# Optimization experiments

Hardware: AMD Instinct MI355X
Metric: run time of the kernel (lower is better)

## Reference

```python
import jax, jax.numpy as jnp
import numpy as np

H = 512
W = 512
TEMP = 256.0
B, S = 4, 4096
C = 2 * H + 2 * W  # pred class dim


def setup_inputs() -> dict:
    key = jax.random.key(0)
    k1, k2, k3, k4, k5 = jax.random.split(key, 5)
    pred = jax.random.normal(k1, (B, S, C), jnp.float32)
    # target columns: [timestamp (sorted), h index, w index, polarity]
    times = jnp.sort(jax.random.uniform(k2, (B, S), jnp.float32, 0.0, 1.0e5), axis=1)
    h_idx = jax.random.randint(k3, (B, S), 0, H).astype(jnp.float32)
    w_idx = jax.random.randint(k4, (B, S), 0, W).astype(jnp.float32)
    p = jax.random.bernoulli(k5, 0.5, (B, S)).astype(jnp.float32)
    target = jnp.stack([times, h_idx, w_idx, p], axis=-1)  # [B,S,4]
    return {"pred": pred, "target": target}


def _soft_ce(pred_logits, tgt_logits):
    # CrossEntropyLoss with soft (probability) targets, reduction='none' -> [B,S]
    return -jnp.sum(jax.nn.softmax(tgt_logits, axis=-1) * jax.nn.log_softmax(pred_logits, axis=-1), axis=-1)


def reference(pred, target):
    t = target[:, :, 0]                      # [B,S] timestamps
    h = target[:, :, 1].astype(jnp.int32)    # [B,S] H indices
    w = target[:, :, 2].astype(jnp.int32)    # [B,S] W indices
    p = target[:, :, 3]                      # [B,S] polarity in {0,1}

    b_ix = jnp.arange(B)[:, None]
    s_ix = jnp.arange(S)[None, :]
    # scatter one-hot targets into a single [B,S,2H+2W] buffer (4 disjoint segments)
    a = jnp.zeros((B, S, C), pred.dtype)
    a = a.at[b_ix, s_ix, h].set(1.0 - p)             # H_0 segment [0,H)
    a = a.at[b_ix, s_ix, H + h].set(p)               # H_1 segment [H,2H)
    a = a.at[b_ix, s_ix, 2 * H + w].set(1.0 - p)     # W_0 segment [2H,2H+W)
    a = a.at[b_ix, s_ix, 2 * H + W + w].set(p)       # W_1 segment [2H+W,2H+2W)

    # decay[j] = exp(-(t[j+1]-t[j])/T); pad last step (unused, carry starts at 0)
    decay = jnp.exp(-(t[:, 1:] - t[:, :-1]) / TEMP)             # [B,S-1]
    decay = jnp.concatenate([decay, jnp.zeros((B, 1), decay.dtype)], axis=1)  # [B,S]

    # reverse linear recurrence: r[j] = a[j] + decay[j] * r[j+1]
    a_t = jnp.swapaxes(a, 0, 1)                 # [S,B,C]
    d_t = jnp.swapaxes(decay, 0, 1)[:, :, None]  # [S,B,1]

    def step(carry, xs):
        ai, di = xs
        r = ai + di * carry
        return r, r

    _, r = jax.lax.scan(step, jnp.zeros((B, C), pred.dtype), (a_t, d_t), reverse=True)
    r = jnp.swapaxes(r, 0, 1)                   # [B,S,C]
    # torch loop is range(S-1, 1, -1): index 0 is never accumulated into
    r = r.at[:, 0, :].set(a[:, 0, :])

    lH0 = _soft_ce(pred[:, :, :H], r[:, :, :H])
    lH1 = _soft_ce(pred[:, :, H:2 * H], r[:, :, H:2 * H])
    lW0 = _soft_ce(pred[:, :, 2 * H:2 * H + W], r[:, :, 2 * H:2 * H + W])
    lW1 = _soft_ce(pred[:, :, 2 * H + W:], r[:, :, 2 * H + W:])

    loss = ((lH0 + lW0) * (1.0 - p) + (lH1 + lW1) * p).mean()
    return loss
```

## Files before the change

kernel.cpp:

```cpp
#include <hip/hip_runtime.h>
#include <math.h>

#define NC 2048
#define NB 4
#define NS 4096
#define INV_TEMP (1.0f / 256.0f)
#define LOG2E 1.44269504088896340736f
#define CL 16
#define NCH (NS / CL)
#define P1_NG 16
#define P1_GS (NS / P1_NG)
#define P1_GC (P1_GS / CL)
#define LOSS_NBLK (NB * NCH)

typedef float f32x4 __attribute__((ext_vector_type(4)));
typedef float f32x2 __attribute__((ext_vector_type(2)));

#define WAVE_SUM_DPP(x)                                                       \
    asm volatile("s_nop 1\n\t"                                                \
                 "v_add_f32 %0, %0, %0 row_shr:1 bound_ctrl:0" : "+v"(x));    \
    asm volatile("s_nop 1\n\t"                                                \
                 "v_add_f32 %0, %0, %0 row_shr:2 bound_ctrl:0" : "+v"(x));    \
    asm volatile("s_nop 1\n\t"                                                \
                 "v_add_f32 %0, %0, %0 row_shr:4 bound_ctrl:0" : "+v"(x));    \
    asm volatile("s_nop 1\n\t"                                                \
                 "v_add_f32 %0, %0, %0 row_shr:8 bound_ctrl:0" : "+v"(x));    \
    asm volatile("s_nop 1\n\t"                                                \
                 "v_add_f32 %0, %0, %0 row_bcast:15 row_mask:0xa" : "+v"(x)); \
    asm volatile("s_nop 1\n\t"                                                \
                 "v_add_f32 %0, %0, %0 row_bcast:31 row_mask:0xc" : "+v"(x));

__device__ __forceinline__ float wave_total(float x)
{
    return __uint_as_float(__builtin_amdgcn_readlane(__float_as_uint(x), 63));
}

__global__ __launch_bounds__(512) void tdl_scan_kernel(
    const float* __restrict__ target, float* __restrict__ rstart)
{
    const int b     = blockIdx.x >> 6;
    const int ctile = blockIdx.x & 63;
    const int tid = threadIdx.x;
    const int ci  = tid & 31;
    const int g   = tid >> 5;

    __shared__ float shbuf[NS * 4];
    __shared__ float shL[P1_NG][32];
    __shared__ float shG[P1_NG];
    f32x4* ev = (f32x4*)shbuf;
    f32x2* pk = (f32x2*)shbuf;

    const int  seg    = ctile >> 4;
    const bool useH   = (seg < 2);
    const float segPar = (float)(seg & 1);
    const float crel  = (float)(((ctile & 15) << 5) + ci);

    const float* tb = target + (size_t)b * NS * 4;

#pragma unroll
    for (int m = 0; m < 8; ++m) {
        int s = m * 512 + tid;
        ev[s] = *((const f32x4*)tb + s);
    }
    __syncthreads();

    float dec_r[8], enc_r[8];
#pragma unroll
    for (int m = 0; m < 8; ++m) {
        int s = m * 512 + tid;
        f32x4 e = ev[s];
        dec_r[m] = (s == NS - 1) ? 0.0f
                  : __expf(-(ev[s + 1].x - e.x) * INV_TEMP);
        enc_r[m] = (e.w == segPar) ? (useH ? e.y : e.z) : -1.0f;
    }
    float alp[P1_GC];
    {
        const int gs = g * P1_GS;
#pragma unroll
        for (int q = 0; q < P1_GC; ++q) {
            int se = gs + q * CL;
            alp[q] = (g == P1_NG - 1 && q == P1_GC - 1) ? 0.0f
                     : __expf(-(ev[se + CL].x - ev[se].x) * INV_TEMP);
        }
        if (ci == 0) {
            shG[g] = (g == P1_NG - 1) ? 0.0f
                     : __expf(-(ev[gs + P1_GS].x - ev[gs].x) * INV_TEMP);
        }
    }
    __syncthreads();

#pragma unroll
    for (int m = 0; m < 8; ++m) {
        int s = m * 512 + tid;
        f32x2 v; v.x = dec_r[m]; v.y = enc_r[m];
        pk[s] = v;
    }
    __syncthreads();

    float cs[P1_GC];
    {
        const int gs = g * P1_GS;
#pragma unroll
        for (int q = P1_GC - 1; q >= 0; --q) {
            float v = 0.0f;
            const int base = gs + q * CL;
#pragma unroll
            for (int i = CL - 1; i >= 0; --i) {
                f32x2 e = pk[base + i];
                v = fmaf(v, e.x, (e.y == crel) ? 1.0f : 0.0f);
            }
            cs[q] = v;
        }
    }

    float L = 0.0f;
#pragma unroll
    for (int q = P1_GC - 1; q >= 0; --q) L = fmaf(alp[q], L, cs[q]);
    shL[g][ci] = L;
    __syncthreads();

    float X = 0.0f;
#pragma unroll
    for (int j = P1_NG - 1; j >= 1; --j)
        if (j > g) X = fmaf(shG[j], X, shL[j][ci]);

    float* rs = rstart + ((size_t)b * NCH + g * P1_GC) * NC + (ctile * 32 + ci);
    float carry = X;
#pragma unroll
    for (int q = P1_GC - 1; q >= 0; --q) {
        carry = fmaf(alp[q], carry, cs[q]);
        rs[(size_t)q * NC] = carry;
    }
}

__global__ __launch_bounds__(256) void tdl_loss_kernel(
    const float* __restrict__ pred, const float* __restrict__ target,
    const float* __restrict__ rstart, float* __restrict__ partials)
{
    const int blk = blockIdx.x;
    const int b = blk >> 8;
    const int k = blk & (NCH - 1);
    const int s0 = k * CL;
    const int tid = threadIdx.x;
    const int wv  = (tid >> 6) & 1;
    const int rh  = tid >> 7;
    const int ln  = tid & 63;

    __shared__ f32x4 ev[CL];
    __shared__ float sh4[4];

    if (tid < CL) {
        const float* tg = target + ((size_t)b * NS + s0 + tid) * 4;
        float t0 = tg[0];
        int s = s0 + tid;
        float dec = (s == NS - 1 || s == 0) ? 0.0f
                   : __expf(-(tg[4] - t0) * INV_TEMP);
        f32x4 e; e.x = dec; e.y = tg[3]; e.z = tg[1]; e.w = tg[2];
        ev[tid] = e;
    }
    __syncthreads();

    const int lc   = ln * 4;
    const int segA = wv * 2;
    const size_t pbase = (size_t)b * NS * NC;

    float vA[8], vB[8];
    if (k == NCH - 1) {
#pragma unroll
        for (int j = 0; j < 8; ++j) { vA[j] = 0.0f; vB[j] = 0.0f; }
    } else {
        const float* rrow = rstart + ((size_t)b * NCH + k + 1) * NC;
#pragma unroll
        for (int q = 0; q < 2; ++q) {
            f32x4 ra = *(const f32x4*)(rrow + segA * 512 + q * 256 + lc);
            f32x4 rb = *(const f32x4*)(rrow + (segA + 1) * 512 + q * 256 + lc);
#pragma unroll
            for (int j = 0; j < 4; ++j) {
                vA[q*4+j] = ra[j] * LOG2E;
                vB[q*4+j] = rb[j] * LOG2E;
            }
        }
    }

    if (rh) {
#pragma unroll
        for (int i = CL - 1; i >= CL / 2; --i) {
            f32x4 e = ev[i];
            const float d    = e.x;
            const float pv   = e.y;
            const float idxf = wv ? e.w : e.z;
            const float aA = (1.0f - pv) * LOG2E;
            const float aB = pv * LOG2E;
#pragma unroll
            for (int q = 0; q < 2; ++q) {
#pragma unroll
                for (int j = 0; j < 4; ++j) {
                    const int id = q * 4 + j;
                    const float myc = (float)(q * 256 + lc + j);
                    const bool m = (idxf == myc);
                    vA[id] = fmaf(vA[id], d, m ? aA : 0.0f);
                    vB[id] = fmaf(vB[id], d, m ? aB : 0.0f);
                }
            }
        }
    }

    const int itop = rh ? (CL / 2 - 1) : (CL - 1);

    f32x4 pf0[2], pf1[2];
    {
        const int paT = (int)ev[itop].y;
        const float* pr = pred + pbase + (size_t)(s0 + itop) * NC
                          + (segA + paT) * 512 + lc;
        pf0[0] = *(const f32x4*)pr; pf0[1] = *(const f32x4*)(pr + 256);
        const int paU = (int)ev[itop - 1].y;
        const float* pr2 = pred + pbase + (size_t)(s0 + itop - 1) * NC
                           + (segA + paU) * 512 + lc;
        pf1[0] = *(const f32x4*)pr2; pf1[1] = *(const f32x4*)(pr2 + 256);
    }

    float acc = 0.0f;
#pragma unroll
    for (int r = 0; r < 8; ++r) {
        const int i = itop - r;
        f32x4 cur[2];
        cur[0] = pf0[0]; cur[1] = pf0[1];
        pf0[0] = pf1[0]; pf0[1] = pf1[1];
        if (r < 6) {
            const int pa = (int)ev[i - 2].y;
            const float* pr = pred + pbase + (size_t)(s0 + i - 2) * NC
                              + (segA + pa) * 512 + lc;
            pf1[0] = *(const f32x4*)pr; pf1[1] = *(const f32x4*)(pr + 256);
        }

        f32x4 e = ev[i];
        const float d    = e.x;
        const float pv   = e.y;
        const float idxf = wv ? e.w : e.z;
        const float aA = (1.0f - pv) * LOG2E;
        const float aB = pv * LOG2E;

        float ser = 0.0f, dot = 0.0f, sep = 0.0f;
#pragma unroll
        for (int q = 0; q < 2; ++q) {
#pragma unroll
            for (int j = 0; j < 4; ++j) {
                const int id = q * 4 + j;
                const float myc = (float)(q * 256 + lc + j);
                const bool m = (idxf == myc);
                vA[id] = fmaf(vA[id], d, m ? aA : 0.0f);
                vB[id] = fmaf(vB[id], d, m ? aB : 0.0f);
                const float vs = (pv != 0.0f) ? vB[id] : vA[id];
                const float ex = exp2f(vs);
                const float pj = cur[q][j];
                ser += ex;
                dot = fmaf(ex, pj, dot);
                sep += __expf(pj);
            }
        }

        WAVE_SUM_DPP(ser)
        WAVE_SUM_DPP(dot)
        WAVE_SUM_DPP(sep)
        const float serT = wave_total(ser);
        const float dotT = wave_total(dot);
        const float sepT = wave_total(sep);
        acc += __logf(sepT) - dotT * __builtin_amdgcn_rcpf(serT);
    }

    if (ln == 0) sh4[tid >> 6] = acc;
    __syncthreads();
    if (tid == 0) partials[blk] = sh4[0] + sh4[1] + sh4[2] + sh4[3];
}

__global__ __launch_bounds__(256) void tdl_reduce_kernel(
    const float* __restrict__ partials, float* __restrict__ out)
{
    const int tid = threadIdx.x;
    __shared__ float sh4[4];

    float s = 0.0f;
#pragma unroll
    for (int i = 0; i < LOSS_NBLK / 256; ++i)
        s += partials[i * 256 + tid];
#pragma unroll
    for (int off = 32; off > 0; off >>= 1)
        s += __shfl_xor(s, off, 64);
    if ((tid & 63) == 0) sh4[tid >> 6] = s;
    __syncthreads();
    if (tid == 0)
        out[0] = (sh4[0] + sh4[1] + sh4[2] + sh4[3])
                 * (1.0f / ((float)NB * (float)NS));
}

extern "C" void kernel_launch(void* const* d_in, const int* in_sizes, int n_in,
                              void* d_out, int out_size, void* d_ws, size_t ws_size,
                              hipStream_t stream)
{
    const float* pred   = (const float*)d_in[0];
    const float* target = (const float*)d_in[1];
    float* out    = (float*)d_out;
    float* rstart = (float*)d_ws;
    float* partials = rstart + (size_t)NB * NCH * NC;

    tdl_scan_kernel<<<NB * 64, 512, 0, stream>>>(target, rstart);
    tdl_loss_kernel<<<NB * NCH, 256, 0, stream>>>(pred, target, rstart, partials);
    tdl_reduce_kernel<<<1, 256, 0, stream>>>(partials, out);
}
```

Before: 31.00 us.

## Store chunk-boundary carries in bf16 and deepen pred prefetch to four rows

The scan kernel now writes the per-chunk recurrence start values as bf16 instead of fp32, and the loss kernel widens them back to float. This halves the intermediate workspace traffic between the two kernels, at the cost of reduced precision in the soft-target logits. Separately, the loss kernel's pred prefetch ring grows from two rows to four, raising memory-level parallelism at the cost of more registers.

Result: slower. 32.29 us (+4.2%).

```diff
diff --git a/kernel.cpp b/kernel.cpp
--- a/kernel.cpp
+++ b/kernel.cpp
@@ -15,6 +15,7 @@
 
 typedef float f32x4 __attribute__((ext_vector_type(4)));
 typedef float f32x2 __attribute__((ext_vector_type(2)));
+typedef unsigned short u16x4 __attribute__((ext_vector_type(4)));
 
 #define WAVE_SUM_DPP(x)                                                       \
     asm volatile("s_nop 1\n\t"                                                \
@@ -35,8 +36,17 @@
     return __uint_as_float(__builtin_amdgcn_readlane(__float_as_uint(x), 63));
 }
 
+__device__ __forceinline__ unsigned short to_bf16(float f)
+{
+    return (unsigned short)((__float_as_uint(f) + 0x8000u) >> 16);
+}
+__device__ __forceinline__ float from_bf16(unsigned short u)
+{
+    return __uint_as_float((unsigned)u << 16);
+}
+
 __global__ __launch_bounds__(512) void tdl_scan_kernel(
-    const float* __restrict__ target, float* __restrict__ rstart)
+    const float* __restrict__ target, unsigned short* __restrict__ rstart)
 {
     const int b     = blockIdx.x >> 6;
     const int ctile = blockIdx.x & 63;
@@ -124,18 +134,19 @@
     for (int j = P1_NG - 1; j >= 1; --j)
         if (j > g) X = fmaf(shG[j], X, shL[j][ci]);
 
-    float* rs = rstart + ((size_t)b * NCH + g * P1_GC) * NC + (ctile * 32 + ci);
+    unsigned short* rs = rstart + ((size_t)b * NCH + g * P1_GC) * NC
+                         + (ctile * 32 + ci);
     float carry = X;
 #pragma unroll
     for (int q = P1_GC - 1; q >= 0; --q) {
         carry = fmaf(alp[q], carry, cs[q]);
-        rs[(size_t)q * NC] = carry;
+        rs[(size_t)q * NC] = to_bf16(carry);
     }
 }
 
 __global__ __launch_bounds__(256) void tdl_loss_kernel(
     const float* __restrict__ pred, const float* __restrict__ target,
-    const float* __restrict__ rstart, float* __restrict__ partials)
+    const unsigned short* __restrict__ rstart, float* __restrict__ partials)
 {
     const int blk = blockIdx.x;
     const int b = blk >> 8;
@@ -169,15 +180,15 @@
 #pragma unroll
         for (int j = 0; j < 8; ++j) { vA[j] = 0.0f; vB[j] = 0.0f; }
     } else {
-        const float* rrow = rstart + ((size_t)b * NCH + k + 1) * NC;
+        const unsigned short* rrow = rstart + ((size_t)b * NCH + k + 1) * NC;
 #pragma unroll
         for (int q = 0; q < 2; ++q) {
-            f32x4 ra = *(const f32x4*)(rrow + segA * 512 + q * 256 + lc);
-            f32x4 rb = *(const f32x4*)(rrow + (segA + 1) * 512 + q * 256 + lc);
+            u16x4 ra = *(const u16x4*)(rrow + segA * 512 + q * 256 + lc);
+            u16x4 rb = *(const u16x4*)(rrow + (segA + 1) * 512 + q * 256 + lc);
 #pragma unroll
             for (int j = 0; j < 4; ++j) {
-                vA[q*4+j] = ra[j] * LOG2E;
-                vB[q*4+j] = rb[j] * LOG2E;
+                vA[q*4+j] = from_bf16(ra[j]) * LOG2E;
+                vB[q*4+j] = from_bf16(rb[j]) * LOG2E;
             }
         }
     }
@@ -207,30 +218,27 @@
 
     const int itop = rh ? (CL / 2 - 1) : (CL - 1);
 
-    f32x4 pf0[2], pf1[2];
-    {
-        const int paT = (int)ev[itop].y;
-        const float* pr = pred + pbase + (size_t)(s0 + itop) * NC
-                          + (segA + paT) * 512 + lc;
-        pf0[0] = *(const f32x4*)pr; pf0[1] = *(const f32x4*)(pr + 256);
-        const int paU = (int)ev[itop - 1].y;
-        const float* pr2 = pred + pbase + (size_t)(s0 + itop - 1) * NC
-                           + (segA + paU) * 512 + lc;
-        pf1[0] = *(const f32x4*)pr2; pf1[1] = *(const f32x4*)(pr2 + 256);
+    f32x4 pf[4][2];
+#pragma unroll
+    for (int d0 = 0; d0 < 4; ++d0) {
+        const int pa = (int)ev[itop - d0].y;
+        const float* pr = pred + pbase + (size_t)(s0 + itop - d0) * NC
+                          + (segA + pa) * 512 + lc;
+        pf[d0][0] = *(const f32x4*)pr;
+        pf[d0][1] = *(const f32x4*)(pr + 256);
     }
 
     float acc = 0.0f;
 #pragma unroll
     for (int r = 0; r < 8; ++r) {
         const int i = itop - r;
-        f32x4 cur[2];
-        cur[0] = pf0[0]; cur[1] = pf0[1];
-        pf0[0] = pf1[0]; pf0[1] = pf1[1];
-        if (r < 6) {
-            const int pa = (int)ev[i - 2].y;
-            const float* pr = pred + pbase + (size_t)(s0 + i - 2) * NC
+        f32x4 cur0 = pf[r & 3][0], cur1 = pf[r & 3][1];
+        if (r < 4) {
+            const int pa = (int)ev[i - 4].y;
+            const float* pr = pred + pbase + (size_t)(s0 + i - 4) * NC
                               + (segA + pa) * 512 + lc;
-            pf1[0] = *(const f32x4*)pr; pf1[1] = *(const f32x4*)(pr + 256);
+            pf[r & 3][0] = *(const f32x4*)pr;
+            pf[r & 3][1] = *(const f32x4*)(pr + 256);
         }
 
         f32x4 e = ev[i];
@@ -243,6 +251,7 @@
         float ser = 0.0f, dot = 0.0f, sep = 0.0f;
 #pragma unroll
         for (int q = 0; q < 2; ++q) {
+            const f32x4 cq = q ? cur1 : cur0;
 #pragma unroll
             for (int j = 0; j < 4; ++j) {
                 const int id = q * 4 + j;
@@ -252,7 +261,7 @@
                 vB[id] = fmaf(vB[id], d, m ? aB : 0.0f);
                 const float vs = (pv != 0.0f) ? vB[id] : vA[id];
                 const float ex = exp2f(vs);
-                const float pj = cur[q][j];
+                const float pj = cq[j];
                 ser += ex;
                 dot = fmaf(ex, pj, dot);
                 sep += __expf(pj);
@@ -299,9 +308,9 @@
 {
     const float* pred   = (const float*)d_in[0];
     const float* target = (const float*)d_in[1];
-    float* out    = (float*)d_out;
-    float* rstart = (float*)d_ws;
-    float* partials = rstart + (size_t)NB * NCH * NC;
+    float* out = (float*)d_out;
+    unsigned short* rstart = (unsigned short*)d_ws;
+    float* partials = (float*)(rstart + (size_t)NB * NCH * NC);
 
     tdl_scan_kernel<<<NB * 64, 512, 0, stream>>>(target, rstart);
     tdl_loss_kernel<<<NB * NCH, 256, 0, stream>>>(pred, target, rstart, partials);
```
